# Performance work log

Measured on AMD Instinct MI355X. Metric: run time of the kernel, lower is better.

## Reference

```python
import jax, jax.numpy as jnp
import numpy as np

EPS = 1e-5  # torch BatchNorm default


def setup_inputs() -> dict:
    key = jax.random.key(0)
    k1, k2, k3 = jax.random.split(key, 3)
    N, C, T, V, O = 64, 64, 300, 25, 64
    x = jax.random.normal(k1, (N, C, T, V), dtype=jnp.float32)
    # 24 = V-1 convs, each (O, C, 1, 2) -> packed as (V-1, O, C, 2), scaled like conv_init
    W = jax.random.normal(k2, (V - 1, O, C, 2), dtype=jnp.float32) * (1.0 / np.sqrt(2 * C))
    b = jax.random.normal(k3, (V - 1, O), dtype=jnp.float32) * 0.01
    gamma = jnp.ones((O,), dtype=jnp.float32)
    beta = jnp.zeros((O,), dtype=jnp.float32)
    return {"x": x, "W": W, "b": b, "gamma": gamma, "beta": beta}


def reference(x, W, b, gamma, beta):
    # x: (N, C, T, V); W: (V-1, O, C, 2); b: (V-1, O)
    # Math of the original loop: out[..., v] = sum_i W0_i @ x[..., v]
    #   + sum_i W1_i @ x[..., (v+i+1) % V] + sum_i b_i
    V = x.shape[-1]
    W0 = W[..., 0]  # (V-1, O, C)
    W1 = W[..., 1]  # (V-1, O, C)
    # identity-tap term: all W0 share the same column -> sum once
    S0 = W0.sum(axis=0)  # (O, C)
    out = jnp.einsum('oc,nctv->notv', S0, x)
    # circular term: source u = (v+i+1)%V  <=>  i = (u-v-1)%V, valid for u != v
    v_idx = jnp.arange(V)
    off = (v_idx[None, :] - v_idx[:, None] - 1) % V  # (V_target, V_source) -> i, equals V-1 when u==v
    W1p = jnp.concatenate([W1, jnp.zeros_like(W1[:1])], axis=0)  # index V-1 maps to zero (u==v excluded)
    Wg = W1p[off]  # (V, V, O, C), zero on the diagonal
    out = out + jnp.einsum('vuoc,nctu->notv', Wg, x)
    out = out + b.sum(axis=0)[None, :, None, None]
    # BatchNorm2d (training-mode batch stats, biased variance) + ReLU
    mean = out.mean(axis=(0, 2, 3), keepdims=True)
    var = out.var(axis=(0, 2, 3), keepdims=True)
    out = (out - mean) * jax.lax.rsqrt(var + EPS)
    out = out * gamma[None, :, None, None] + beta[None, :, None, None]
    return jax.nn.relu(out)
```

## Files before the change

kernel.cpp:

```cpp
#include <hip/hip_runtime.h>


typedef short  s16x8 __attribute__((ext_vector_type(8)));
typedef float  f32x4 __attribute__((ext_vector_type(4)));

#define NTHR_   256
#define RPB_    250
#define NBR_    30
#define TS_     260

__device__ __forceinline__ unsigned short f2bf(float f) {
  unsigned u = __builtin_bit_cast(unsigned, f);
  return (unsigned short)((u + 0x7FFFu + ((u >> 16) & 1u)) >> 16);
}

__global__ void pack_w_kernel(const float* __restrict__ W, s16x8* __restrict__ Wg) {
  int idx = blockIdx.x * 256 + threadIdx.x;
  if (idx >= 12800) return;
  int lane  = idx & 63;
  int ni    = (idx >> 6) & 3;
  int chunk = (idx >> 8) & 1;
  int s     = idx >> 9;
  int o     = (ni << 4) + (lane & 15);
  int cbase = (chunk << 5) + ((lane >> 4) << 3);
  s16x8 h;
#pragma unroll
  for (int j = 0; j < 8; ++j) {
    int c = cbase + j;
    float val;
    if (s == 0) {
      val = 0.f;
      for (int i = 0; i < 24; ++i) val += W[((i * 64 + o) * 64 + c) * 2];
    } else {
      val = W[(((s - 1) * 64 + o) * 64 + c) * 2 + 1];
    }
    h[j] = (short)f2bf(val);
  }
  Wg[idx] = h;
}

#define ADV(J) { bool w_ = (u[J] == 24); u[J] = w_ ? 0 : u[J] + 1; \
                 aoc[J] += w_ ? -384 : 16; }
#define MM(RT, CT, AF, BF) \
  acc[RT][CT] = __builtin_amdgcn_mfma_f32_16x16x32_bf16(AF, BF, acc[RT][CT], 0, 0, 0);

#define SHIFT(S_, BB)                                                          \
  {                                                                            \
    int sc_ = (S_) + 2; sc_ = (sc_ > 24) ? 24 : sc_;                           \
    const s16x8* ws_ = Wg + sc_ * 512;                                         \
    s16x8 Br0_ = ws_[tid], Br1_ = ws_[256 + tid];                              \
    const char* bq_ = Bsh + (BB) * 8192 + 4096 + (lane << 4);                  \
    __builtin_amdgcn_s_setprio(1);                                             \
    Aq0 = *(const s16x8*)(Ash + aoc[0] + 16384);                               \
    MM(0, 0, Ap0, Bp0) MM(0, 1, Ap0, Bp1)                                      \
    Bq0 = *(const s16x8*)(bq_);                                                \
    MM(0, 2, Ap0, Bp2) MM(0, 3, Ap0, Bp3)                                      \
    Aq1 = *(const s16x8*)(Ash + aoc[1] + 16384);                               \
    MM(1, 0, Ap1, Bp0) MM(1, 1, Ap1, Bp1)                                      \
    Bq1 = *(const s16x8*)(bq_ + 1024);                                         \
    MM(1, 2, Ap1, Bp2) MM(1, 3, Ap1, Bp3)                                      \
    Aq2 = *(const s16x8*)(Ash + aoc[2] + 16384);                               \
    MM(2, 0, Ap2, Bp0) MM(2, 1, Ap2, Bp1)                                      \
    Bq2 = *(const s16x8*)(bq_ + 2048);                                         \
    MM(2, 2, Ap2, Bp2) MM(2, 3, Ap2, Bp3)                                      \
    Aq3 = *(const s16x8*)(Ash + aoc[3] + 16384);                               \
    MM(3, 0, Ap3, Bp0) MM(3, 1, Ap3, Bp1)                                      \
    Bq3 = *(const s16x8*)(bq_ + 3072);                                         \
    MM(3, 2, Ap3, Bp2) MM(3, 3, Ap3, Bp3)                                      \
    __builtin_amdgcn_s_setprio(0);                                             \
    __syncthreads();                                                           \
    const char* bp_ = Bsh + (((BB) ^ 1) * 8192) + (lane << 4);                 \
    __builtin_amdgcn_s_setprio(1);                                             \
    ADV(0) Ap0 = *(const s16x8*)(Ash + aoc[0]);                                \
    MM(0, 0, Aq0, Bq0) MM(0, 1, Aq0, Bq1)                                      \
    Bp0 = *(const s16x8*)(bp_);                                                \
    MM(0, 2, Aq0, Bq2) MM(0, 3, Aq0, Bq3)                                      \
    ADV(1) Ap1 = *(const s16x8*)(Ash + aoc[1]);                                \
    MM(1, 0, Aq1, Bq0) MM(1, 1, Aq1, Bq1)                                      \
    Bp1 = *(const s16x8*)(bp_ + 1024);                                         \
    MM(1, 2, Aq1, Bq2) MM(1, 3, Aq1, Bq3)                                      \
    ADV(2) Ap2 = *(const s16x8*)(Ash + aoc[2]);                                \
    MM(2, 0, Aq2, Bq0) MM(2, 1, Aq2, Bq1)                                      \
    Bp2 = *(const s16x8*)(bp_ + 2048);                                         \
    MM(2, 2, Aq2, Bq2) MM(2, 3, Aq2, Bq3)                                      \
    ADV(3) Ap3 = *(const s16x8*)(Ash + aoc[3]);                                \
    MM(3, 0, Aq3, Bq0) MM(3, 1, Aq3, Bq1)                                      \
    Bp3 = *(const s16x8*)(bp_ + 3072);                                         \
    MM(3, 2, Aq3, Bq2) MM(3, 3, Aq3, Bq3)                                      \
    __builtin_amdgcn_s_setprio(0);                                             \
    *(s16x8*)(Bsh + (BB) * 8192 + (tid << 4)) = Br0_;                          \
    *(s16x8*)(Bsh + (BB) * 8192 + 4096 + (tid << 4)) = Br1_;                   \
  }

__global__ __launch_bounds__(NTHR_, 3) void tap_mm_kernel(
    const float* __restrict__ x, const s16x8* __restrict__ Wg,
    float* __restrict__ out, float* __restrict__ partials) {
  __shared__ __align__(16) char Ash[32768];
  __shared__ __align__(16) char Bsh[16384];
  float* red2 = (float*)Bsh;
  int br = blockIdx.x, n = blockIdx.y;
  int r0 = br * RPB_;
  const float* xn = x + n * 480000 + r0;
  int tid = threadIdx.x;
  int wid = tid >> 6, lane = tid & 63;
  int l15 = lane & 15, lk = lane >> 4;

  s16x8 p0 = Wg[tid], p1 = Wg[256 + tid], p2 = Wg[512 + tid], p3 = Wg[768 + tid];

#pragma unroll 2
  for (int it = 0; it < 8; ++it) {
    bool vld = tid < RPB_;
    s16x8 h;
#pragma unroll
    for (int j = 0; j < 8; ++j) {
      float f = vld ? xn[((it << 3) + j) * 7500 + tid] : 0.f;
      h[j] = (short)f2bf(f);
    }
    *(s16x8*)(Ash + (it << 12) + (tid << 4)) = h;
  }
  *(s16x8*)(Bsh + (tid << 4))         = p0;
  *(s16x8*)(Bsh + 4096 + (tid << 4))  = p1;
  *(s16x8*)(Bsh + 8192 + (tid << 4))  = p2;
  *(s16x8*)(Bsh + 12288 + (tid << 4)) = p3;

  int u[4], aoc[4];
#pragma unroll
  for (int rt = 0; rt < 4; ++rt) {
    int srow = (wid << 6) + (rt << 4) + l15;
    u[rt]   = srow % 25;
    aoc[rt] = (lk << 12) + (srow << 4);
  }
  f32x4 acc[4][4];
#pragma unroll
  for (int rt = 0; rt < 4; ++rt)
#pragma unroll
    for (int ct = 0; ct < 4; ++ct) acc[rt][ct] = (f32x4){0.f, 0.f, 0.f, 0.f};

  __syncthreads();

  s16x8 Ap0 = *(const s16x8*)(Ash + aoc[0]);
  s16x8 Ap1 = *(const s16x8*)(Ash + aoc[1]);
  s16x8 Ap2 = *(const s16x8*)(Ash + aoc[2]);
  s16x8 Ap3 = *(const s16x8*)(Ash + aoc[3]);
  const char* b0_ = Bsh + (lane << 4);
  s16x8 Bp0 = *(const s16x8*)(b0_);
  s16x8 Bp1 = *(const s16x8*)(b0_ + 1024);
  s16x8 Bp2 = *(const s16x8*)(b0_ + 2048);
  s16x8 Bp3 = *(const s16x8*)(b0_ + 3072);
  s16x8 Aq0, Aq1, Aq2, Aq3, Bq0, Bq1, Bq2, Bq3;

  for (int k = 0; k < 12; ++k) {
    SHIFT(2 * k, 0)
    SHIFT(2 * k + 1, 1)
  }
  SHIFT(24, 0)

  __syncthreads();

  float s1v[4] = {0.f, 0.f, 0.f, 0.f}, s2v[4] = {0.f, 0.f, 0.f, 0.f};
#pragma unroll
  for (int rt = 0; rt < 4; ++rt) {
#pragma unroll
    for (int qq = 0; qq < 4; ++qq) {
      int rloc = (wid << 6) + (rt << 4) + (lk << 2) + qq;
      if (rloc < RPB_) {
#pragma unroll
        for (int ct = 0; ct < 4; ++ct) {
          float val = acc[rt][ct][qq];
          s1v[ct] += val;
          s2v[ct] += val * val;
        }
      }
    }
  }
#pragma unroll
  for (int ct = 0; ct < 4; ++ct) {
    float a = s1v[ct], b = s2v[ct];
    a += __shfl_xor(a, 16); a += __shfl_xor(a, 32);
    b += __shfl_xor(b, 16); b += __shfl_xor(b, 32);
    if (lane < 16) {
      int base = ((((wid << 2) + ct) << 4) + l15) * 2;
      red2[base]     = a;
      red2[base + 1] = b;
    }
  }

  float* T = (float*)Ash;
  float* outb = out + n * 480000 + r0;
#pragma unroll
  for (int qt = 0; qt < 4; ++qt) {
    __syncthreads();
#pragma unroll
    for (int rt = 0; rt < 4; ++rt) {
      int row0 = (wid << 6) + (rt << 4) + (lk << 2);
      *(f32x4*)&T[l15 * TS_ + row0] = acc[rt][qt];
    }
    __syncthreads();
    if (qt == 0 && tid < 128) {
      int o = tid >> 1, m = tid & 1;
      int ct = o >> 4, ol = o & 15;
      float sres = 0.f;
#pragma unroll
      for (int w = 0; w < 4; ++w)
        sres += red2[((((w << 2) + ct) << 4) + ol) * 2 + m];
      int bl = n * NBR_ + br;
      partials[bl * 128 + m * 64 + o] = sres;
    }
#pragma unroll
    for (int it = 0; it < 8; ++it) {
      int idx = tid + it * NTHR_;
      if (idx < 2000) {
        int ol = idx / 125, r2 = idx - ol * 125;
        *(float2*)&outb[((qt << 4) + ol) * 7500 + (r2 << 1)] =
            *(float2*)&T[ol * TS_ + (r2 << 1)];
      }
    }
  }
}

__global__ void finalize_kernel(const float* __restrict__ part,
                                const float* __restrict__ gamma,
                                const float* __restrict__ beta,
                                float* __restrict__ scsh) {
  __shared__ float sm[512];
  int o = blockIdx.x;
  int tid = threadIdx.x;
  float s1 = 0.f, s2 = 0.f;
  for (int b = tid; b < 64 * NBR_; b += 256) {
    s1 += part[b * 128 + o];
    s2 += part[b * 128 + 64 + o];
  }
  sm[tid] = s1; sm[256 + tid] = s2;
  __syncthreads();
  for (int st = 128; st >= 1; st >>= 1) {
    if (tid < st) { sm[tid] += sm[tid + st]; sm[256 + tid] += sm[256 + tid + st]; }
    __syncthreads();
  }
  if (tid == 0) {
    const float inv = 1.0f / 480000.0f;
    float mean = sm[0] * inv;
    float var  = sm[256] * inv - mean * mean;
    float sc = gamma[o] * rsqrtf(var + 1e-5f);
    float sh = beta[o] - mean * sc;
    scsh[o]      = sc;
    scsh[64 + o] = sh;
  }
}

__global__ void bn_relu_kernel(float4* __restrict__ out, const float* __restrict__ scsh) {
  int i = blockIdx.x * blockDim.x + threadIdx.x;
  const int total = 7680000;
  int stride = gridDim.x * blockDim.x;
  for (; i < total; i += stride) {
    int o = (i / 1875) & 63;
    float sc = scsh[o], sh = scsh[64 + o];
    float4 v = out[i];
    v.x = fmaxf(fmaf(v.x, sc, sh), 0.f);
    v.y = fmaxf(fmaf(v.y, sc, sh), 0.f);
    v.z = fmaxf(fmaf(v.z, sc, sh), 0.f);
    v.w = fmaxf(fmaf(v.w, sc, sh), 0.f);
    out[i] = v;
  }
}

extern "C" void kernel_launch(void* const* d_in, const int* in_sizes, int n_in,
                              void* d_out, int out_size, void* d_ws, size_t ws_size,
                              hipStream_t stream) {
  const float* x     = (const float*)d_in[0];
  const float* W     = (const float*)d_in[1];
  const float* gamma = (const float*)d_in[3];
  const float* beta  = (const float*)d_in[4];
  float* out = (float*)d_out;

  char* ws = (char*)d_ws;
  s16x8* Wg       = (s16x8*)ws;
  float* partials = (float*)(ws + 204800);
  float* scsh     = (float*)(ws + 204800 + 983040);

  pack_w_kernel<<<dim3(50), dim3(256), 0, stream>>>(W, Wg);
  tap_mm_kernel<<<dim3(NBR_, 64), dim3(NTHR_), 0, stream>>>(x, Wg, out, partials);
  finalize_kernel<<<dim3(64), dim3(256), 0, stream>>>(partials, gamma, beta, scsh);
  bn_relu_kernel<<<dim3(2048), dim3(256), 0, stream>>>((float4*)out, scsh);
}
```

Measured before the change: 172.1 us.

## Halve rows per block and stage weight taps via direct global-to-LDS loads

Rows per block drop from 250 to 125, which doubles the grid to 60x64 blocks, halves LDS for the activation tile and raises the occupancy hint to 4 blocks per CU. Each wave now computes 2 row tiles instead of 4, so register pressure falls. Weight tap staging moves from register round-trips to global_load_lds issued right after the barrier, which is meant to overlap weight fetch with MFMA work. In exchange, each weight slice is loaded by twice as many blocks and per-block overhead grows. Output stores narrow from float2 to scalar floats, and the partials buffer doubles in size.

```diff
diff --git a/kernel.cpp b/kernel.cpp
--- a/kernel.cpp
+++ b/kernel.cpp
@@ -5,14 +5,19 @@
 typedef float  f32x4 __attribute__((ext_vector_type(4)));
 
 #define NTHR_   256
-#define RPB_    250
-#define NBR_    30
-#define TS_     260
+#define RPB_    125
+#define NBR_    60
+#define TS_     132
 
 __device__ __forceinline__ unsigned short f2bf(float f) {
   unsigned u = __builtin_bit_cast(unsigned, f);
   return (unsigned short)((u + 0x7FFFu + ((u >> 16) & 1u)) >> 16);
 }
+
+#define GLDS16(G, L)                                                           \
+  __builtin_amdgcn_global_load_lds(                                            \
+      (const __attribute__((address_space(1))) void*)(G),                      \
+      (__attribute__((address_space(3))) void*)(L), 16, 0, 0);
 
 __global__ void pack_w_kernel(const float* __restrict__ W, s16x8* __restrict__ Wg) {
   int idx = blockIdx.x * 256 + threadIdx.x;
@@ -44,31 +49,31 @@
 #define MM(RT, CT, AF, BF) \
   acc[RT][CT] = __builtin_amdgcn_mfma_f32_16x16x32_bf16(AF, BF, acc[RT][CT], 0, 0, 0);
 
+#define BSTAGE(S_, BB)                                                         \
+  {                                                                            \
+    int sc_ = (S_) + 2; sc_ = (sc_ > 24) ? 24 : sc_;                           \
+    const char* g_ = (const char*)(Wg + sc_ * 512) + goff;                     \
+    GLDS16(g_,        Bsh + (BB) * 8192 + loff)                                \
+    GLDS16(g_ + 1024, Bsh + (BB) * 8192 + loff + 1024)                         \
+  }
+
 #define SHIFT(S_, BB)                                                          \
   {                                                                            \
-    int sc_ = (S_) + 2; sc_ = (sc_ > 24) ? 24 : sc_;                           \
-    const s16x8* ws_ = Wg + sc_ * 512;                                         \
-    s16x8 Br0_ = ws_[tid], Br1_ = ws_[256 + tid];                              \
     const char* bq_ = Bsh + (BB) * 8192 + 4096 + (lane << 4);                  \
     __builtin_amdgcn_s_setprio(1);                                             \
-    Aq0 = *(const s16x8*)(Ash + aoc[0] + 16384);                               \
+    Aq0 = *(const s16x8*)(Ash + aoc[0] + 8192);                                \
     MM(0, 0, Ap0, Bp0) MM(0, 1, Ap0, Bp1)                                      \
     Bq0 = *(const s16x8*)(bq_);                                                \
     MM(0, 2, Ap0, Bp2) MM(0, 3, Ap0, Bp3)                                      \
-    Aq1 = *(const s16x8*)(Ash + aoc[1] + 16384);                               \
+    Aq1 = *(const s16x8*)(Ash + aoc[1] + 8192);                                \
     MM(1, 0, Ap1, Bp0) MM(1, 1, Ap1, Bp1)                                      \
     Bq1 = *(const s16x8*)(bq_ + 1024);                                         \
     MM(1, 2, Ap1, Bp2) MM(1, 3, Ap1, Bp3)                                      \
-    Aq2 = *(const s16x8*)(Ash + aoc[2] + 16384);                               \
-    MM(2, 0, Ap2, Bp0) MM(2, 1, Ap2, Bp1)                                      \
     Bq2 = *(const s16x8*)(bq_ + 2048);                                         \
-    MM(2, 2, Ap2, Bp2) MM(2, 3, Ap2, Bp3)                                      \
-    Aq3 = *(const s16x8*)(Ash + aoc[3] + 16384);                               \
-    MM(3, 0, Ap3, Bp0) MM(3, 1, Ap3, Bp1)                                      \
     Bq3 = *(const s16x8*)(bq_ + 3072);                                         \
-    MM(3, 2, Ap3, Bp2) MM(3, 3, Ap3, Bp3)                                      \
     __builtin_amdgcn_s_setprio(0);                                             \
     __syncthreads();                                                           \
+    BSTAGE(S_, BB)                                                             \
     const char* bp_ = Bsh + (((BB) ^ 1) * 8192) + (lane << 4);                 \
     __builtin_amdgcn_s_setprio(1);                                             \
     ADV(0) Ap0 = *(const s16x8*)(Ash + aoc[0]);                                \
@@ -79,23 +84,15 @@
     MM(1, 0, Aq1, Bq0) MM(1, 1, Aq1, Bq1)                                      \
     Bp1 = *(const s16x8*)(bp_ + 1024);                                         \
     MM(1, 2, Aq1, Bq2) MM(1, 3, Aq1, Bq3)                                      \
-    ADV(2) Ap2 = *(const s16x8*)(Ash + aoc[2]);                                \
-    MM(2, 0, Aq2, Bq0) MM(2, 1, Aq2, Bq1)                                      \
     Bp2 = *(const s16x8*)(bp_ + 2048);                                         \
-    MM(2, 2, Aq2, Bq2) MM(2, 3, Aq2, Bq3)                                      \
-    ADV(3) Ap3 = *(const s16x8*)(Ash + aoc[3]);                                \
-    MM(3, 0, Aq3, Bq0) MM(3, 1, Aq3, Bq1)                                      \
     Bp3 = *(const s16x8*)(bp_ + 3072);                                         \
-    MM(3, 2, Aq3, Bq2) MM(3, 3, Aq3, Bq3)                                      \
     __builtin_amdgcn_s_setprio(0);                                             \
-    *(s16x8*)(Bsh + (BB) * 8192 + (tid << 4)) = Br0_;                          \
-    *(s16x8*)(Bsh + (BB) * 8192 + 4096 + (tid << 4)) = Br1_;                   \
-  }
-
-__global__ __launch_bounds__(NTHR_, 3) void tap_mm_kernel(
+  }
+
+__global__ __launch_bounds__(NTHR_, 4) void tap_mm_kernel(
     const float* __restrict__ x, const s16x8* __restrict__ Wg,
     float* __restrict__ out, float* __restrict__ partials) {
-  __shared__ __align__(16) char Ash[32768];
+  __shared__ __align__(16) char Ash[16384];
   __shared__ __align__(16) char Bsh[16384];
   float* red2 = (float*)Bsh;
   int br = blockIdx.x, n = blockIdx.y;
@@ -104,35 +101,42 @@
   int tid = threadIdx.x;
   int wid = tid >> 6, lane = tid & 63;
   int l15 = lane & 15, lk = lane >> 4;
-
-  s16x8 p0 = Wg[tid], p1 = Wg[256 + tid], p2 = Wg[512 + tid], p3 = Wg[768 + tid];
-
-#pragma unroll 2
-  for (int it = 0; it < 8; ++it) {
-    bool vld = tid < RPB_;
+  int loff = wid << 11;
+  int goff = loff + (lane << 4);
+
+  {
+    const char* g0 = (const char*)Wg + goff;
+    GLDS16(g0,        Bsh + loff)
+    GLDS16(g0 + 1024, Bsh + loff + 1024)
+    const char* g1 = (const char*)(Wg + 512) + goff;
+    GLDS16(g1,        Bsh + 8192 + loff)
+    GLDS16(g1 + 1024, Bsh + 8192 + loff + 1024)
+  }
+
+#pragma unroll
+  for (int it = 0; it < 4; ++it) {
+    int id = tid + it * NTHR_;
+    int slot = id >> 7, row = id & 127;
+    bool vld = row < RPB_;
     s16x8 h;
 #pragma unroll
     for (int j = 0; j < 8; ++j) {
-      float f = vld ? xn[((it << 3) + j) * 7500 + tid] : 0.f;
+      float f = vld ? xn[((slot << 3) + j) * 7500 + row] : 0.f;
       h[j] = (short)f2bf(f);
     }
-    *(s16x8*)(Ash + (it << 12) + (tid << 4)) = h;
-  }
-  *(s16x8*)(Bsh + (tid << 4))         = p0;
-  *(s16x8*)(Bsh + 4096 + (tid << 4))  = p1;
-  *(s16x8*)(Bsh + 8192 + (tid << 4))  = p2;
-  *(s16x8*)(Bsh + 12288 + (tid << 4)) = p3;
-
-  int u[4], aoc[4];
-#pragma unroll
-  for (int rt = 0; rt < 4; ++rt) {
-    int srow = (wid << 6) + (rt << 4) + l15;
+    *(s16x8*)(Ash + (id << 4)) = h;
+  }
+
+  int u[2], aoc[2];
+#pragma unroll
+  for (int rt = 0; rt < 2; ++rt) {
+    int srow = (wid << 5) + (rt << 4) + l15;
     u[rt]   = srow % 25;
-    aoc[rt] = (lk << 12) + (srow << 4);
-  }
-  f32x4 acc[4][4];
-#pragma unroll
-  for (int rt = 0; rt < 4; ++rt)
+    aoc[rt] = (lk << 11) + (srow << 4);
+  }
+  f32x4 acc[2][4];
+#pragma unroll
+  for (int rt = 0; rt < 2; ++rt)
 #pragma unroll
     for (int ct = 0; ct < 4; ++ct) acc[rt][ct] = (f32x4){0.f, 0.f, 0.f, 0.f};
 
@@ -140,14 +144,12 @@
 
   s16x8 Ap0 = *(const s16x8*)(Ash + aoc[0]);
   s16x8 Ap1 = *(const s16x8*)(Ash + aoc[1]);
-  s16x8 Ap2 = *(const s16x8*)(Ash + aoc[2]);
-  s16x8 Ap3 = *(const s16x8*)(Ash + aoc[3]);
   const char* b0_ = Bsh + (lane << 4);
   s16x8 Bp0 = *(const s16x8*)(b0_);
   s16x8 Bp1 = *(const s16x8*)(b0_ + 1024);
   s16x8 Bp2 = *(const s16x8*)(b0_ + 2048);
   s16x8 Bp3 = *(const s16x8*)(b0_ + 3072);
-  s16x8 Aq0, Aq1, Aq2, Aq3, Bq0, Bq1, Bq2, Bq3;
+  s16x8 Aq0, Aq1, Bq0, Bq1, Bq2, Bq3;
 
   for (int k = 0; k < 12; ++k) {
     SHIFT(2 * k, 0)
@@ -159,10 +161,10 @@
 
   float s1v[4] = {0.f, 0.f, 0.f, 0.f}, s2v[4] = {0.f, 0.f, 0.f, 0.f};
 #pragma unroll
-  for (int rt = 0; rt < 4; ++rt) {
+  for (int rt = 0; rt < 2; ++rt) {
 #pragma unroll
     for (int qq = 0; qq < 4; ++qq) {
-      int rloc = (wid << 6) + (rt << 4) + (lk << 2) + qq;
+      int rloc = (wid << 5) + (rt << 4) + (lk << 2) + qq;
       if (rloc < RPB_) {
 #pragma unroll
         for (int ct = 0; ct < 4; ++ct) {
@@ -191,8 +193,8 @@
   for (int qt = 0; qt < 4; ++qt) {
     __syncthreads();
 #pragma unroll
-    for (int rt = 0; rt < 4; ++rt) {
-      int row0 = (wid << 6) + (rt << 4) + (lk << 2);
+    for (int rt = 0; rt < 2; ++rt) {
+      int row0 = (wid << 5) + (rt << 4) + (lk << 2);
       *(f32x4*)&T[l15 * TS_ + row0] = acc[rt][qt];
     }
     __syncthreads();
@@ -210,9 +212,8 @@
     for (int it = 0; it < 8; ++it) {
       int idx = tid + it * NTHR_;
       if (idx < 2000) {
-        int ol = idx / 125, r2 = idx - ol * 125;
-        *(float2*)&outb[((qt << 4) + ol) * 7500 + (r2 << 1)] =
-            *(float2*)&T[ol * TS_ + (r2 << 1)];
+        int ol = idx / 125, row = idx - ol * 125;
+        outb[((qt << 4) + ol) * 7500 + row] = T[ol * TS_ + row];
       }
     }
   }
@@ -275,7 +276,7 @@
   char* ws = (char*)d_ws;
   s16x8* Wg       = (s16x8*)ws;
   float* partials = (float*)(ws + 204800);
-  float* scsh     = (float*)(ws + 204800 + 983040);
+  float* scsh     = (float*)(ws + 204800 + 1966080);
 
   pack_w_kernel<<<dim3(50), dim3(256), 0, stream>>>(W, Wg);
   tap_mm_kernel<<<dim3(NBR_, 64), dim3(NTHR_), 0, stream>>>(x, Wg, out, partials);
```

Measured after the change: 181.5 us. +5.4%, slower.
